# Performance work log

Measured on AMD Instinct MI355X. Metric: run time of the kernel, lower is better.

The kernel has to match this reference:

```python
import jax, jax.numpy as jnp
import numpy as np

D_MODEL = 256
D_STATE = 64
D_CONV = 4
EXPAND = 2
HEADDIM = 64
D_INNER = EXPAND * D_MODEL            # 512
NHEADS = D_INNER // HEADDIM           # 8
D_XBC = D_INNER + 2 * D_STATE         # 640 (x, B, C; ngroups=1)
D_IN_PROJ = 2 * D_INNER + 2 * D_STATE + NHEADS  # 1160


def setup_inputs() -> dict:
    key = jax.random.key(0)
    ks = jax.random.split(key, 8)
    x = jax.random.normal(ks[0], (64, 5000, 12), jnp.float32)
    W_in = jax.random.normal(ks[1], (D_MODEL, D_IN_PROJ), jnp.float32) * 0.02
    conv_w = jax.random.normal(ks[2], (D_XBC, D_CONV), jnp.float32) * 0.1
    conv_b = jnp.zeros((D_XBC,), jnp.float32)
    A_log = jnp.log(jax.random.uniform(ks[3], (NHEADS,), jnp.float32, 1.0, 16.0))
    dt_bias = jax.random.normal(ks[4], (NHEADS,), jnp.float32) * 0.1
    D = jnp.ones((NHEADS,), jnp.float32)
    norm_w = jnp.ones((D_INNER,), jnp.float32)
    W_out = jax.random.normal(ks[5], (D_INNER, D_MODEL), jnp.float32) * 0.02
    return {"x": x, "W_in": W_in, "conv_w": conv_w, "conv_b": conv_b,
            "A_log": A_log, "dt_bias": dt_bias, "D": D,
            "norm_w": norm_w, "W_out": W_out}


def _mamba2(u, W_in, conv_w, conv_b, A_log, dt_bias, D, norm_w, W_out):
    b, l, _ = u.shape
    zxbcdt = u @ W_in                                   # (b,l,1160)
    z = zxbcdt[..., :D_INNER]                           # (b,l,512)
    xBC = zxbcdt[..., D_INNER:D_INNER + D_XBC]          # (b,l,640)
    dt = zxbcdt[..., D_INNER + D_XBC:]                  # (b,l,8)
    # causal depthwise conv1d (kernel 4) + SiLU
    xp = jnp.pad(xBC, ((0, 0), (D_CONV - 1, 0), (0, 0)))
    xBC = sum(xp[:, k:k + l, :] * conv_w[:, k] for k in range(D_CONV)) + conv_b
    xBC = jax.nn.silu(xBC)
    xs = xBC[..., :D_INNER].reshape(b, l, NHEADS, HEADDIM)
    Bm = xBC[..., D_INNER:D_INNER + D_STATE]            # (b,l,64)
    Cm = xBC[..., D_INNER + D_STATE:]                   # (b,l,64)
    dt = jax.nn.softplus(dt + dt_bias)                  # (b,l,h)
    A = -jnp.exp(A_log)                                 # (h,)

    def step(h, inp):
        x_t, dt_t, B_t, C_t = inp                       # (b,h,p),(b,h),(b,n),(b,n)
        decay = jnp.exp(dt_t * A)                       # (b,h)
        h = h * decay[..., None, None] + (dt_t[..., None] * x_t)[..., None] * B_t[:, None, None, :]
        y = jnp.einsum('bhpn,bn->bhp', h, C_t)
        return h, y

    h0 = jnp.zeros((b, NHEADS, HEADDIM, D_STATE), u.dtype)
    _, ys = jax.lax.scan(step, h0, (xs.transpose(1, 0, 2, 3), dt.transpose(1, 0, 2),
                                    Bm.transpose(1, 0, 2), Cm.transpose(1, 0, 2)))
    y = ys.transpose(1, 0, 2, 3) + D[None, None, :, None] * xs   # D skip, per head
    y = y.reshape(b, l, D_INNER)
    # RMSNormGated: gate then rmsnorm
    y = y * jax.nn.silu(z)
    y = y * jax.lax.rsqrt(jnp.mean(y * y, axis=-1, keepdims=True) + 1e-5) * norm_w
    return y @ W_out                                    # (b,l,256)


def reference(x, W_in, conv_w, conv_b, A_log, dt_bias, D, norm_w, W_out):
    b = x.shape[0]
    u = x.reshape(b, 250, 240)                          # 'b (t p1) f -> b t (p1 f)'
    u = jnp.pad(u, ((0, 0), (0, 0), (0, D_MODEL - 240)))
    y = _mamba2(u, W_in, conv_w, conv_b, A_log, dt_bias, D, norm_w, W_out)
    y = jax.nn.selu(y)                                  # AlphaDropout is identity at eval
    y = y[..., :240]
    return y.reshape(b, 5000, 12)
```

## Files before the change

### kernel.cpp

```cpp
#include <hip/hip_runtime.h>
#include <cstdint>
#include <cstddef>

#define D_MODEL 256
#define D_STATE 64
#define HEADDIM 64
#define D_INNER 512
#define NHEADS 8
#define D_XBC 640
#define NPROJ 1160
#define BATCH 64
#define SEQ 250
#define ROWS (BATCH * SEQ)
#define KIN 240
#define KPAD 256
#define NPAD 1216
#define TPAD 256

typedef __bf16 bf16x8 __attribute__((ext_vector_type(8)));
typedef float f32x4 __attribute__((ext_vector_type(4)));

__device__ __forceinline__ float readlane_f(float v, int lane) {
    return __uint_as_float(__builtin_amdgcn_readlane(__float_as_uint(v), lane));
}
__device__ __forceinline__ float silu_f(float x) { return x * (1.f / (1.f + __expf(-x))); }
__device__ __forceinline__ unsigned short bf16_rne(float f) {
    unsigned int u = __float_as_uint(f);
    u += 0x7fff + ((u >> 16) & 1);
    return (unsigned short)(u >> 16);
}
__device__ __forceinline__ float bf2f(unsigned short u) {
    return __uint_as_float(((unsigned int)u) << 16);
}
__device__ __forceinline__ unsigned int pack2(float a, float b) {
    return (unsigned int)bf16_rne(a) | ((unsigned int)bf16_rne(b) << 16);
}

__global__ __launch_bounds__(256) void cast_kernel(const float* __restrict__ x,
                                                   const float* __restrict__ Win,
                                                   unsigned short* __restrict__ a_bf,
                                                   unsigned short* __restrict__ bt_bf) {
    int idx = blockIdx.x * 256 + threadIdx.x;
    const int NA = ROWS * KPAD;
    if (idx < NA) {
        int row = idx >> 8, c = idx & 255;
        float v = (c < KIN) ? x[row * KIN + c] : 0.f;
        a_bf[idx] = bf16_rne(v);
    } else if (idx < NA + NPAD * KPAD) {
        int r = idx - NA;
        int n = r >> 8, k = r & 255;
        float v = (n < NPROJ && k < KIN) ? Win[k * NPROJ + n] : 0.f;
        bt_bf[r] = bf16_rne(v);
    }
}

#define SA 40
__global__ __launch_bounds__(256) void gemm1_mfma(const unsigned short* __restrict__ A,
                                                  const unsigned short* __restrict__ Bt,
                                                  float* __restrict__ C) {
    __shared__ unsigned short As[128 * SA];
    __shared__ unsigned short Bs[64 * SA];
    const int tid = threadIdx.x;
    const int lane = tid & 63, wave = tid >> 6;
    const int wm = wave >> 1, wn = wave & 1;
    const int q = lane >> 4, l15 = lane & 15;
    const int rowBase = blockIdx.y * 128, colBase = blockIdx.x * 64;
    f32x4 acc[4][2] = {};

    const int sr = tid >> 2;
    const int sc = (tid & 3) * 8;

    for (int k0 = 0; k0 < KPAD; k0 += 32) {
        *(float4*)&As[sr * SA + sc] =
            *(const float4*)&A[(size_t)(rowBase + sr) * KPAD + k0 + sc];
        *(float4*)&As[(sr + 64) * SA + sc] =
            *(const float4*)&A[(size_t)(rowBase + sr + 64) * KPAD + k0 + sc];
        *(float4*)&Bs[sr * SA + sc] =
            *(const float4*)&Bt[(size_t)(colBase + sr) * KPAD + k0 + sc];
        __syncthreads();

        bf16x8 bfr[2];
#pragma unroll
        for (int nt = 0; nt < 2; nt++)
            bfr[nt] = *(const bf16x8*)&Bs[(wn * 32 + nt * 16 + l15) * SA + q * 8];
#pragma unroll
        for (int mt = 0; mt < 4; mt++) {
            bf16x8 afr = *(const bf16x8*)&As[(wm * 64 + mt * 16 + l15) * SA + q * 8];
#pragma unroll
            for (int nt = 0; nt < 2; nt++)
                acc[mt][nt] = __builtin_amdgcn_mfma_f32_16x16x32_bf16(afr, bfr[nt],
                                                                      acc[mt][nt], 0, 0, 0);
        }
        __syncthreads();
    }
#pragma unroll
    for (int mt = 0; mt < 4; mt++) {
        int grow = rowBase + wm * 64 + mt * 16 + q * 4;
#pragma unroll
        for (int nt = 0; nt < 2; nt++) {
            int gcol = colBase + wn * 32 + nt * 16 + l15;
            if (gcol < NPROJ) {
#pragma unroll
                for (int reg = 0; reg < 4; reg++)
                    C[(size_t)(grow + reg) * NPROJ + gcol] = acc[mt][nt][reg];
            }
        }
    }
}

#define CT_IN_STR 68
#define CT_TR_STR 70
__global__ __launch_bounds__(256) void conv_kernel(const float* __restrict__ zxbcdt,
                                                   const float* __restrict__ conv_w,
                                                   const float* __restrict__ conv_b,
                                                   const float* __restrict__ dt_bias,
                                                   unsigned short* __restrict__ xc_bf,
                                                   unsigned short* __restrict__ xcT_bf,
                                                   float* __restrict__ dtp) {
    const int b = blockIdx.x;
    const int t0 = blockIdx.z * 64;
    if (blockIdx.y == 10) {
        for (int it = threadIdx.x; it < 512; it += 256) {
            int h = it & 7, ts = it >> 3;
            int t = t0 + (ts << 1);
            t = t0 + (it >> 3);
            if (t < SEQ) {
                float v = zxbcdt[(size_t)(b * SEQ + t) * NPROJ + D_INNER + D_XBC + h] +
                          dt_bias[h];
                dtp[(size_t)(b * SEQ + t) * NHEADS + h] =
                    (v > 20.f) ? v : __logf(1.f + __expf(v));
            }
        }
        return;
    }
    __shared__ float In[67 * CT_IN_STR];
    __shared__ unsigned short OutT[64 * CT_TR_STR];
    const int cg = blockIdx.y;
    const int tid = threadIdx.x;
    const int lane = tid & 63;
    const int w = tid >> 6;
    const int ch = cg * 64 + lane;

    for (int r = w; r < 67; r += 4) {
        int t = t0 - 3 + r;
        float v = (t >= 0 && t < SEQ)
                      ? zxbcdt[(size_t)(b * SEQ + t) * NPROJ + D_INNER + ch]
                      : 0.f;
        In[r * CT_IN_STR + lane] = v;
    }
    __syncthreads();
    const float w0 = conv_w[ch * 4 + 0], w1 = conv_w[ch * 4 + 1];
    const float w2 = conv_w[ch * 4 + 2], w3 = conv_w[ch * 4 + 3];
    const float bias = conv_b[ch];
    unsigned short vals[16];
#pragma unroll
    for (int i = 0; i < 16; i++) {
        int tt = w * 16 + i;
        float acc = fmaf(w3, In[(tt + 3) * CT_IN_STR + lane],
                    fmaf(w2, In[(tt + 2) * CT_IN_STR + lane],
                    fmaf(w1, In[(tt + 1) * CT_IN_STR + lane],
                    fmaf(w0, In[tt * CT_IN_STR + lane], bias))));
        float sv = silu_f(acc);
        unsigned short bv = (t0 + tt < SEQ) ? bf16_rne(sv) : (unsigned short)0;
        vals[i] = bv;
        OutT[lane * CT_TR_STR + tt] = bv;
    }
#pragma unroll
    for (int i = 0; i < 16; i++) {
        int tt = w * 16 + i;
        if (t0 + tt < SEQ)
            xc_bf[(size_t)(b * SEQ + t0 + tt) * D_XBC + ch] = vals[i];
    }
    __syncthreads();
    unsigned short* dstbase = xcT_bf + ((size_t)b * D_XBC + cg * 64) * TPAD + t0;
#pragma unroll
    for (int i = 0; i < 16; i++) {
        int c2 = w * 16 + i;
        dstbase[(size_t)c2 * TPAD + lane] = OutT[c2 * CT_TR_STR + lane];
    }
}

#define LSTR 72
__global__ __launch_bounds__(256) void scan_intra(const unsigned short* __restrict__ xc_bf,
                                                  const unsigned short* __restrict__ xcT_bf,
                                                  const float* __restrict__ dtp,
                                                  const float* __restrict__ A_log,
                                                  const float* __restrict__ Dvec,
                                                  unsigned short* __restrict__ yout_bf,
                                                  unsigned short* __restrict__ st_g) {
    __shared__ unsigned short C_l[64 * LSTR];
    __shared__ unsigned short BP_l[64 * LSTR];
    __shared__ unsigned short XT_l[64 * LSTR];
    __shared__ float cs_s[64], dts_s[64], fws_s[64];

    const int blk = blockIdx.x;
    const int bh = blk >> 2, c = blk & 3;
    const int b = bh >> 3, h = bh & 7;
    const int tid = threadIdx.x;
    const int lane = tid & 63, w = tid >> 6;
    const int q = lane >> 4, l15 = lane & 15;
    const int t0 = c * 64;
    const float A = -__expf(A_log[h]);
    const float Dh = Dvec[h];

    const int r = tid >> 2, c0 = (tid & 3) * 16;

    {
        if (t0 + r < SEQ) {
            const unsigned short* rowp = xc_bf + (size_t)(b * SEQ + t0 + r) * D_XBC;
            *(uint4*)&C_l[r * LSTR + c0] = *(const uint4*)&rowp[D_INNER + D_STATE + c0];
            *(uint4*)&C_l[r * LSTR + c0 + 8] =
                *(const uint4*)&rowp[D_INNER + D_STATE + c0 + 8];
            *(uint4*)&BP_l[r * LSTR + c0] = *(const uint4*)&rowp[D_INNER + c0];
            *(uint4*)&BP_l[r * LSTR + c0 + 8] = *(const uint4*)&rowp[D_INNER + c0 + 8];
        } else {
            uint4 z = {0, 0, 0, 0};
            *(uint4*)&C_l[r * LSTR + c0] = z;
            *(uint4*)&C_l[r * LSTR + c0 + 8] = z;
            *(uint4*)&BP_l[r * LSTR + c0] = z;
            *(uint4*)&BP_l[r * LSTR + c0 + 8] = z;
        }
        const unsigned short* xrow =
            xcT_bf + ((size_t)b * D_XBC + h * HEADDIM + r) * TPAD + t0;
        *(uint4*)&XT_l[r * LSTR + c0] = *(const uint4*)&xrow[c0];
        *(uint4*)&XT_l[r * LSTR + c0 + 8] = *(const uint4*)&xrow[c0 + 8];
    }
    uint4 braw0, braw1;
    {
        const unsigned short* brow =
            xcT_bf + ((size_t)b * D_XBC + D_INNER + r) * TPAD + t0 + c0;
        braw0 = *(const uint4*)&brow[0];
        braw1 = *(const uint4*)&brow[8];
    }
    if (w == 0) {
        int t = lane;
        float dtv = (t0 + t < SEQ) ? dtp[(size_t)(b * SEQ + t0 + t) * NHEADS + h] : 0.f;
        float csv = dtv * A;
#pragma unroll
        for (int o = 1; o < 64; o <<= 1) {
            float u = __shfl_up(csv, o, 64);
            if (lane >= o) csv += u;
        }
        float tot = readlane_f(csv, 63);
        cs_s[t] = csv;
        dts_s[t] = dtv;
        fws_s[t] = dtv * __expf(tot - csv);
    }
    __syncthreads();

    f32x4 g[4] = {};
#pragma unroll
    for (int k0 = 0; k0 < 64; k0 += 32) {
        bf16x8 ca = *(const bf16x8*)&C_l[(w * 16 + l15) * LSTR + k0 + q * 8];
#pragma unroll
        for (int nt = 0; nt < 4; nt++) {
            bf16x8 bb = *(const bf16x8*)&BP_l[(nt * 16 + l15) * LSTR + k0 + q * 8];
            g[nt] = __builtin_amdgcn_mfma_f32_16x16x32_bf16(ca, bb, g[nt], 0, 0, 0);
        }
    }
    __syncthreads();

    {
        unsigned short tmp[16];
        const unsigned short* rp = (const unsigned short*)&braw0;
#pragma unroll
        for (int j = 0; j < 8; j++) tmp[j] = bf16_rne(bf2f(rp[j]) * fws_s[c0 + j]);
        rp = (const unsigned short*)&braw1;
#pragma unroll
        for (int j = 0; j < 8; j++) tmp[8 + j] = bf16_rne(bf2f(rp[j]) * fws_s[c0 + 8 + j]);
        *(uint4*)&C_l[r * LSTR + c0] = *(uint4*)&tmp[0];
        *(uint4*)&C_l[r * LSTR + c0 + 8] = *(uint4*)&tmp[8];
    }
#pragma unroll
    for (int nt = 0; nt < 4; nt++) {
#pragma unroll
        for (int rr = 0; rr < 4; rr++) {
            int t = w * 16 + q * 4 + rr;
            int s = nt * 16 + l15;
            float pv = 0.f;
            if (s <= t) {
                pv = g[nt][rr] * __expf(cs_s[t] - cs_s[s]) * dts_s[s];
                if (s == t) pv += Dh;
            }
            unsigned int u = bf16_rne(pv);
            unsigned int partner = (unsigned int)__shfl_xor((int)u, 1, 64);
            if ((l15 & 1) == 0)
                *(unsigned int*)&BP_l[t * LSTR + nt * 16 + l15] = u | (partner << 16);
        }
    }
    __syncthreads();

    f32x4 y[4] = {};
#pragma unroll
    for (int k0 = 0; k0 < 64; k0 += 32) {
        bf16x8 pa = *(const bf16x8*)&BP_l[(w * 16 + l15) * LSTR + k0 + q * 8];
#pragma unroll
        for (int nt = 0; nt < 4; nt++) {
            bf16x8 xb = *(const bf16x8*)&XT_l[(nt * 16 + l15) * LSTR + k0 + q * 8];
            y[nt] = __builtin_amdgcn_mfma_f32_16x16x32_bf16(pa, xb, y[nt], 0, 0, 0);
        }
    }
    if (c < 3) {
        f32x4 st[4] = {};
#pragma unroll
        for (int k0 = 0; k0 < 64; k0 += 32) {
            bf16x8 xa = *(const bf16x8*)&XT_l[(w * 16 + l15) * LSTR + k0 + q * 8];
#pragma unroll
            for (int nt = 0; nt < 4; nt++) {
                bf16x8 bwb = *(const bf16x8*)&C_l[(nt * 16 + l15) * LSTR + k0 + q * 8];
                st[nt] = __builtin_amdgcn_mfma_f32_16x16x32_bf16(xa, bwb, st[nt], 0, 0, 0);
            }
        }
        unsigned short* stc = st_g + ((size_t)(bh * 3 + c)) * 4096;
#pragma unroll
        for (int nt = 0; nt < 4; nt++)
#pragma unroll
            for (int rr = 0; rr < 4; rr++) {
                unsigned int u = bf16_rne(st[nt][rr]);
                unsigned int partner = (unsigned int)__shfl_xor((int)u, 1, 64);
                if ((l15 & 1) == 0)
                    *(unsigned int*)&stc[(w * 16 + q * 4 + rr) * 64 + nt * 16 + l15] =
                        u | (partner << 16);
            }
    }
#pragma unroll
    for (int nt = 0; nt < 4; nt++)
#pragma unroll
        for (int rr = 0; rr < 4; rr++) {
            int t = w * 16 + q * 4 + rr;
            if (t0 + t < SEQ) {
                int p = nt * 16 + l15;
                unsigned int u = bf16_rne(y[nt][rr]);
                unsigned int partner = (unsigned int)__shfl_xor((int)u, 1, 64);
                if ((l15 & 1) == 0)
                    *(unsigned int*)&yout_bf[(size_t)(b * SEQ + t0 + t) * D_INNER +
                                             h * HEADDIM + p] = u | (partner << 16);
            }
        }
}

__global__ __launch_bounds__(256) void scan_inter(const unsigned short* __restrict__ xc_bf,
                                                  const float* __restrict__ dtp,
                                                  const float* __restrict__ A_log,
                                                  unsigned short* __restrict__ yout_bf,
                                                  const unsigned short* __restrict__ st_g) {
    __shared__ unsigned short C_l[64 * LSTR];
    __shared__ unsigned short h_l[64 * LSTR];
    __shared__ float cs_s[64];
    __shared__ float csum[4];

    const int blk = blockIdx.x;
    const int bh = blk / 3, c = (blk - bh * 3) + 1;
    const int b = bh >> 3, h = bh & 7;
    const int tid = threadIdx.x;
    const int lane = tid & 63, w = tid >> 6;
    const int q = lane >> 4, l15 = lane & 15;
    const int t0 = c * 64;
    const float A = -__expf(A_log[h]);

    {
        int t = lane;
        int gt = w * 64 + t;
        float dtv = (gt < SEQ) ? dtp[(size_t)(b * SEQ + gt) * NHEADS + h] : 0.f;
        float csv = dtv * A;
#pragma unroll
        for (int o = 1; o < 64; o <<= 1) {
            float u = __shfl_up(csv, o, 64);
            if (lane >= o) csv += u;
        }
        if (w == c) cs_s[t] = csv;
        if (lane == 63) csum[w] = csv;
    }
    {
        int r = tid >> 2, c0 = (tid & 3) * 16;
        if (t0 + r < SEQ) {
            const unsigned short* rowp = xc_bf + (size_t)(b * SEQ + t0 + r) * D_XBC;
            *(uint4*)&C_l[r * LSTR + c0] = *(const uint4*)&rowp[D_INNER + D_STATE + c0];
            *(uint4*)&C_l[r * LSTR + c0 + 8] =
                *(const uint4*)&rowp[D_INNER + D_STATE + c0 + 8];
        } else {
            uint4 z = {0, 0, 0, 0};
            *(uint4*)&C_l[r * LSTR + c0] = z;
            *(uint4*)&C_l[r * LSTR + c0 + 8] = z;
        }
    }
    __syncthreads();

    {
        float wgt[3];
        for (int cp = 0; cp < c; cp++) {
            float s = 0.f;
            for (int j = cp + 1; j < c; j++) s += csum[j];
            wgt[cp] = __expf(s);
        }
        const unsigned short* stb = st_g + (size_t)bh * 3 * 4096;
        for (int i = tid; i < 4096; i += 256) {
            float acc = 0.f;
            for (int cp = 0; cp < c; cp++) acc += wgt[cp] * bf2f(stb[cp * 4096 + i]);
            h_l[(i >> 6) * LSTR + (i & 63)] = bf16_rne(acc);
        }
    }
    __syncthreads();

    f32x4 in[4] = {};
#pragma unroll
    for (int k0 = 0; k0 < 64; k0 += 32) {
        bf16x8 ca = *(const bf16x8*)&C_l[(w * 16 + l15) * LSTR + k0 + q * 8];
#pragma unroll
        for (int nt = 0; nt < 4; nt++) {
            bf16x8 hb = *(const bf16x8*)&h_l[(nt * 16 + l15) * LSTR + k0 + q * 8];
            in[nt] = __builtin_amdgcn_mfma_f32_16x16x32_bf16(ca, hb, in[nt], 0, 0, 0);
        }
    }
#pragma unroll
    for (int nt = 0; nt < 4; nt++)
#pragma unroll
        for (int r = 0; r < 4; r++) {
            int t = w * 16 + q * 4 + r;
            if (t0 + t < SEQ) {
                int p = nt * 16 + l15;
                size_t ai = (size_t)(b * SEQ + t0 + t) * D_INNER + h * HEADDIM + p;
                float alpha = __expf(cs_s[t]);
                float nv = bf2f(yout_bf[ai]) + alpha * in[nt][r];
                unsigned int u = bf16_rne(nv);
                unsigned int partner = (unsigned int)__shfl_xor((int)u, 1, 64);
                if ((l15 & 1) == 0)
                    *(unsigned int*)&yout_bf[ai] = u | (partner << 16);
            }
        }
}

__global__ __launch_bounds__(256) void wcast_kernel(const float* __restrict__ Wout,
                                                    unsigned short* __restrict__ wt_bf) {
    int idx = blockIdx.x * 256 + threadIdx.x;
    int n = idx & 255, k = idx >> 8;
    wt_bf[n * D_INNER + k] = bf16_rne(Wout[k * D_MODEL + n]);
}

__global__ __launch_bounds__(256) void gate_kernel(const unsigned short* __restrict__ yout_bf,
                                                   const float* __restrict__ zx,
                                                   const float* __restrict__ norm_w,
                                                   unsigned short* __restrict__ g_bf) {
    const int wid = threadIdx.x >> 6, lane = threadIdx.x & 63;
    const int row = blockIdx.x * 4 + wid;
    const unsigned short* yr = yout_bf + (size_t)row * D_INNER;
    const float* zr = zx + (size_t)row * NPROJ;
    const int c0 = lane * 8;
    uint4 yp = *(const uint4*)&yr[c0];
    float4 z0 = *(const float4*)&zr[c0], z1 = *(const float4*)&zr[c0 + 4];
    float g[8];
    g[0] = bf2f((unsigned short)(yp.x & 0xffff)) * silu_f(z0.x);
    g[1] = bf2f((unsigned short)(yp.x >> 16)) * silu_f(z0.y);
    g[2] = bf2f((unsigned short)(yp.y & 0xffff)) * silu_f(z0.z);
    g[3] = bf2f((unsigned short)(yp.y >> 16)) * silu_f(z0.w);
    g[4] = bf2f((unsigned short)(yp.z & 0xffff)) * silu_f(z1.x);
    g[5] = bf2f((unsigned short)(yp.z >> 16)) * silu_f(z1.y);
    g[6] = bf2f((unsigned short)(yp.w & 0xffff)) * silu_f(z1.z);
    g[7] = bf2f((unsigned short)(yp.w >> 16)) * silu_f(z1.w);
    float s = 0.f;
#pragma unroll
    for (int i = 0; i < 8; i++) s = fmaf(g[i], g[i], s);
#pragma unroll
    for (int o = 32; o; o >>= 1) s += __shfl_xor(s, o, 64);
    float rms = rsqrtf(s * (1.f / 512.f) + 1e-5f);
    float4 w0 = *(const float4*)&norm_w[c0], w1 = *(const float4*)&norm_w[c0 + 4];
    uint4 pk;
    pk.x = pack2(g[0] * rms * w0.x, g[1] * rms * w0.y);
    pk.y = pack2(g[2] * rms * w0.z, g[3] * rms * w0.w);
    pk.z = pack2(g[4] * rms * w1.x, g[5] * rms * w1.y);
    pk.w = pack2(g[6] * rms * w1.z, g[7] * rms * w1.w);
    *(uint4*)&g_bf[(size_t)row * D_INNER + c0] = pk;
}

__global__ __launch_bounds__(256) void gemm2_mfma(const unsigned short* __restrict__ A,
                                                  const unsigned short* __restrict__ Bt,
                                                  float* __restrict__ out) {
    __shared__ unsigned short As[128 * SA];
    __shared__ unsigned short Bs[64 * SA];
    const int tid = threadIdx.x;
    const int lane = tid & 63, wave = tid >> 6;
    const int wm = wave >> 1, wn = wave & 1;
    const int q = lane >> 4, l15 = lane & 15;
    const int rowBase = blockIdx.y * 128, colBase = blockIdx.x * 64;
    f32x4 acc[4][2] = {};

    const int sr = tid >> 2;
    const int sc = (tid & 3) * 8;

    for (int k0 = 0; k0 < D_INNER; k0 += 32) {
        *(float4*)&As[sr * SA + sc] =
            *(const float4*)&A[(size_t)(rowBase + sr) * D_INNER + k0 + sc];
        *(float4*)&As[(sr + 64) * SA + sc] =
            *(const float4*)&A[(size_t)(rowBase + sr + 64) * D_INNER + k0 + sc];
        *(float4*)&Bs[sr * SA + sc] =
            *(const float4*)&Bt[(size_t)(colBase + sr) * D_INNER + k0 + sc];
        __syncthreads();

        bf16x8 bfr[2];
#pragma unroll
        for (int nt = 0; nt < 2; nt++)
            bfr[nt] = *(const bf16x8*)&Bs[(wn * 32 + nt * 16 + l15) * SA + q * 8];
#pragma unroll
        for (int mt = 0; mt < 4; mt++) {
            bf16x8 afr = *(const bf16x8*)&As[(wm * 64 + mt * 16 + l15) * SA + q * 8];
#pragma unroll
            for (int nt = 0; nt < 2; nt++)
                acc[mt][nt] = __builtin_amdgcn_mfma_f32_16x16x32_bf16(afr, bfr[nt],
                                                                      acc[mt][nt], 0, 0, 0);
        }
        __syncthreads();
    }
    const float SC = 1.0507009873554805f, AL = 1.6732632423543772f;
#pragma unroll
    for (int mt = 0; mt < 4; mt++) {
        int grow = rowBase + wm * 64 + mt * 16 + q * 4;
#pragma unroll
        for (int nt = 0; nt < 2; nt++) {
            int gcol = colBase + wn * 32 + nt * 16 + l15;
            if (gcol < 240) {
#pragma unroll
                for (int reg = 0; reg < 4; reg++) {
                    float v = acc[mt][nt][reg];
                    v = (v > 0.f) ? SC * v : SC * AL * (__expf(v) - 1.f);
                    out[(size_t)(grow + reg) * 240 + gcol] = v;
                }
            }
        }
    }
}

extern "C" void kernel_launch(void* const* d_in, const int* in_sizes, int n_in,
                              void* d_out, int out_size, void* d_ws, size_t ws_size,
                              hipStream_t stream) {
    const float* x = (const float*)d_in[0];
    const float* W_in = (const float*)d_in[1];
    const float* conv_w = (const float*)d_in[2];
    const float* conv_b = (const float*)d_in[3];
    const float* A_log = (const float*)d_in[4];
    const float* dt_bias = (const float*)d_in[5];
    const float* Dv = (const float*)d_in[6];
    const float* norm_w = (const float*)d_in[7];
    const float* W_out = (const float*)d_in[8];
    float* out = (float*)d_out;

    float* ws = (float*)d_ws;
    float* zxbcdt = ws;
    unsigned short* xc_bf = (unsigned short*)(zxbcdt + (size_t)ROWS * NPROJ);
    unsigned short* xcT_bf = xc_bf + (size_t)ROWS * D_XBC;
    float* dtp = (float*)(xcT_bf + (size_t)BATCH * D_XBC * TPAD);
    unsigned short* yout_bf = (unsigned short*)(dtp + (size_t)ROWS * NHEADS);
    unsigned short* st_g = yout_bf + (size_t)ROWS * D_INNER;

    unsigned short* a_bf = xc_bf;
    unsigned short* bt_bf = a_bf + (size_t)ROWS * KPAD;
    unsigned short* wt_bf = (unsigned short*)dtp;
    unsigned short* g_bf = xc_bf;

    int cast_total = ROWS * KPAD + NPAD * KPAD;
    cast_kernel<<<dim3((cast_total + 255) / 256), 256, 0, stream>>>(x, W_in, a_bf, bt_bf);

    gemm1_mfma<<<dim3(NPAD / 64, ROWS / 128), 256, 0, stream>>>(a_bf, bt_bf, zxbcdt);

    conv_kernel<<<dim3(BATCH, 11, 4), 256, 0, stream>>>(zxbcdt, conv_w, conv_b, dt_bias,
                                                        xc_bf, xcT_bf, dtp);

    scan_intra<<<dim3(BATCH * NHEADS * 4), 256, 0, stream>>>(xc_bf, xcT_bf, dtp, A_log, Dv,
                                                             yout_bf, st_g);

    scan_inter<<<dim3(BATCH * NHEADS * 3), 256, 0, stream>>>(xc_bf, dtp, A_log,
                                                             yout_bf, st_g);

    wcast_kernel<<<dim3(D_INNER * D_MODEL / 256), 256, 0, stream>>>(W_out, wt_bf);

    gate_kernel<<<dim3(ROWS / 4), 256, 0, stream>>>(yout_bf, zxbcdt, norm_w, g_bf);

    gemm2_mfma<<<dim3(D_MODEL / 64, ROWS / 128), 256, 0, stream>>>(g_bf, wt_bf, out);
}
```

Baseline: 222.6 us.

## Fuse input cast into GEMM1 and store projection output as bf16

Drops the separate activation cast kernel: GEMM1 now reads the fp32 input directly and converts it to bf16 while staging into shared memory, zero-padding K beyond 240. The z/xBC part of the projection output is written as packed bf16 with row stride 1152, and the dt columns go to a separate small fp32 buffer. Conv and gate kernels are changed to read the bf16 tensor. This roughly halves the intermediate write and read traffic, at the cost of bf16 rounding of z and xBC before conv and gating, plus a lane shuffle in the GEMM epilogue.

```diff
diff --git a/kernel.cpp b/kernel.cpp
--- a/kernel.cpp
+++ b/kernel.cpp
@@ -9,6 +9,7 @@
 #define NHEADS 8
 #define D_XBC 640
 #define NPROJ 1160
+#define ZXW 1152
 #define BATCH 64
 #define SEQ 250
 #define ROWS (BATCH * SEQ)
@@ -36,28 +37,19 @@
     return (unsigned int)bf16_rne(a) | ((unsigned int)bf16_rne(b) << 16);
 }
 
-__global__ __launch_bounds__(256) void cast_kernel(const float* __restrict__ x,
-                                                   const float* __restrict__ Win,
-                                                   unsigned short* __restrict__ a_bf,
-                                                   unsigned short* __restrict__ bt_bf) {
+__global__ __launch_bounds__(256) void cast_w_kernel(const float* __restrict__ Win,
+                                                     unsigned short* __restrict__ bt_bf) {
     int idx = blockIdx.x * 256 + threadIdx.x;
-    const int NA = ROWS * KPAD;
-    if (idx < NA) {
-        int row = idx >> 8, c = idx & 255;
-        float v = (c < KIN) ? x[row * KIN + c] : 0.f;
-        a_bf[idx] = bf16_rne(v);
-    } else if (idx < NA + NPAD * KPAD) {
-        int r = idx - NA;
-        int n = r >> 8, k = r & 255;
-        float v = (n < NPROJ && k < KIN) ? Win[k * NPROJ + n] : 0.f;
-        bt_bf[r] = bf16_rne(v);
-    }
+    int n = idx >> 8, k = idx & 255;
+    float v = (n < NPROJ && k < KIN) ? Win[k * NPROJ + n] : 0.f;
+    bt_bf[idx] = bf16_rne(v);
 }
 
 #define SA 40
-__global__ __launch_bounds__(256) void gemm1_mfma(const unsigned short* __restrict__ A,
+__global__ __launch_bounds__(256) void gemm1_mfma(const float* __restrict__ X,
                                                   const unsigned short* __restrict__ Bt,
-                                                  float* __restrict__ C) {
+                                                  unsigned short* __restrict__ Czx,
+                                                  float* __restrict__ dtraw) {
     __shared__ unsigned short As[128 * SA];
     __shared__ unsigned short Bs[64 * SA];
     const int tid = threadIdx.x;
@@ -71,10 +63,34 @@
     const int sc = (tid & 3) * 8;
 
     for (int k0 = 0; k0 < KPAD; k0 += 32) {
-        *(float4*)&As[sr * SA + sc] =
-            *(const float4*)&A[(size_t)(rowBase + sr) * KPAD + k0 + sc];
-        *(float4*)&As[(sr + 64) * SA + sc] =
-            *(const float4*)&A[(size_t)(rowBase + sr + 64) * KPAD + k0 + sc];
+        const int kseg = k0 + sc;
+        const bool kv = kseg < KIN;
+        {
+            unsigned short tmp[8] = {0, 0, 0, 0, 0, 0, 0, 0};
+            if (kv) {
+                const float* xr = X + (size_t)(rowBase + sr) * KIN + kseg;
+                float4 a = *(const float4*)&xr[0];
+                float4 b2 = *(const float4*)&xr[4];
+                tmp[0] = bf16_rne(a.x); tmp[1] = bf16_rne(a.y);
+                tmp[2] = bf16_rne(a.z); tmp[3] = bf16_rne(a.w);
+                tmp[4] = bf16_rne(b2.x); tmp[5] = bf16_rne(b2.y);
+                tmp[6] = bf16_rne(b2.z); tmp[7] = bf16_rne(b2.w);
+            }
+            *(uint4*)&As[sr * SA + sc] = *(uint4*)tmp;
+        }
+        {
+            unsigned short tmp[8] = {0, 0, 0, 0, 0, 0, 0, 0};
+            if (kv) {
+                const float* xr = X + (size_t)(rowBase + sr + 64) * KIN + kseg;
+                float4 a = *(const float4*)&xr[0];
+                float4 b2 = *(const float4*)&xr[4];
+                tmp[0] = bf16_rne(a.x); tmp[1] = bf16_rne(a.y);
+                tmp[2] = bf16_rne(a.z); tmp[3] = bf16_rne(a.w);
+                tmp[4] = bf16_rne(b2.x); tmp[5] = bf16_rne(b2.y);
+                tmp[6] = bf16_rne(b2.z); tmp[7] = bf16_rne(b2.w);
+            }
+            *(uint4*)&As[(sr + 64) * SA + sc] = *(uint4*)tmp;
+        }
         *(float4*)&Bs[sr * SA + sc] =
             *(const float4*)&Bt[(size_t)(colBase + sr) * KPAD + k0 + sc];
         __syncthreads();
@@ -95,14 +111,23 @@
     }
 #pragma unroll
     for (int mt = 0; mt < 4; mt++) {
-        int grow = rowBase + wm * 64 + mt * 16 + q * 4;
+        int grow0 = rowBase + wm * 64 + mt * 16 + q * 4;
 #pragma unroll
         for (int nt = 0; nt < 2; nt++) {
             int gcol = colBase + wn * 32 + nt * 16 + l15;
-            if (gcol < NPROJ) {
+            if (gcol < ZXW) {
+#pragma unroll
+                for (int reg = 0; reg < 4; reg++) {
+                    unsigned int u = bf16_rne(acc[mt][nt][reg]);
+                    unsigned int partner = (unsigned int)__shfl_xor((int)u, 1, 64);
+                    if ((l15 & 1) == 0)
+                        *(unsigned int*)&Czx[(size_t)(grow0 + reg) * ZXW + gcol] =
+                            u | (partner << 16);
+                }
+            } else if (gcol < NPROJ) {
 #pragma unroll
                 for (int reg = 0; reg < 4; reg++)
-                    C[(size_t)(grow + reg) * NPROJ + gcol] = acc[mt][nt][reg];
+                    dtraw[(size_t)(grow0 + reg) * NHEADS + (gcol - ZXW)] = acc[mt][nt][reg];
             }
         }
     }
@@ -110,7 +135,8 @@
 
 #define CT_IN_STR 68
 #define CT_TR_STR 70
-__global__ __launch_bounds__(256) void conv_kernel(const float* __restrict__ zxbcdt,
+__global__ __launch_bounds__(256) void conv_kernel(const unsigned short* __restrict__ zxbc,
+                                                   const float* __restrict__ dtraw,
                                                    const float* __restrict__ conv_w,
                                                    const float* __restrict__ conv_b,
                                                    const float* __restrict__ dt_bias,
@@ -121,12 +147,10 @@
     const int t0 = blockIdx.z * 64;
     if (blockIdx.y == 10) {
         for (int it = threadIdx.x; it < 512; it += 256) {
-            int h = it & 7, ts = it >> 3;
-            int t = t0 + (ts << 1);
-            t = t0 + (it >> 3);
+            int h = it & 7;
+            int t = t0 + (it >> 3);
             if (t < SEQ) {
-                float v = zxbcdt[(size_t)(b * SEQ + t) * NPROJ + D_INNER + D_XBC + h] +
-                          dt_bias[h];
+                float v = dtraw[(size_t)(b * SEQ + t) * NHEADS + h] + dt_bias[h];
                 dtp[(size_t)(b * SEQ + t) * NHEADS + h] =
                     (v > 20.f) ? v : __logf(1.f + __expf(v));
             }
@@ -144,7 +168,7 @@
     for (int r = w; r < 67; r += 4) {
         int t = t0 - 3 + r;
         float v = (t >= 0 && t < SEQ)
-                      ? zxbcdt[(size_t)(b * SEQ + t) * NPROJ + D_INNER + ch]
+                      ? bf2f(zxbc[(size_t)(b * SEQ + t) * ZXW + D_INNER + ch])
                       : 0.f;
         In[r * CT_IN_STR + lane] = v;
     }
@@ -438,25 +462,21 @@
 }
 
 __global__ __launch_bounds__(256) void gate_kernel(const unsigned short* __restrict__ yout_bf,
-                                                   const float* __restrict__ zx,
+                                                   const unsigned short* __restrict__ zxbc,
                                                    const float* __restrict__ norm_w,
                                                    unsigned short* __restrict__ g_bf) {
     const int wid = threadIdx.x >> 6, lane = threadIdx.x & 63;
     const int row = blockIdx.x * 4 + wid;
     const unsigned short* yr = yout_bf + (size_t)row * D_INNER;
-    const float* zr = zx + (size_t)row * NPROJ;
+    const unsigned short* zr = zxbc + (size_t)row * ZXW;
     const int c0 = lane * 8;
     uint4 yp = *(const uint4*)&yr[c0];
-    float4 z0 = *(const float4*)&zr[c0], z1 = *(const float4*)&zr[c0 + 4];
+    uint4 zp = *(const uint4*)&zr[c0];
+    const unsigned short* ys = (const unsigned short*)&yp;
+    const unsigned short* zs = (const unsigned short*)&zp;
     float g[8];
-    g[0] = bf2f((unsigned short)(yp.x & 0xffff)) * silu_f(z0.x);
-    g[1] = bf2f((unsigned short)(yp.x >> 16)) * silu_f(z0.y);
-    g[2] = bf2f((unsigned short)(yp.y & 0xffff)) * silu_f(z0.z);
-    g[3] = bf2f((unsigned short)(yp.y >> 16)) * silu_f(z0.w);
-    g[4] = bf2f((unsigned short)(yp.z & 0xffff)) * silu_f(z1.x);
-    g[5] = bf2f((unsigned short)(yp.z >> 16)) * silu_f(z1.y);
-    g[6] = bf2f((unsigned short)(yp.w & 0xffff)) * silu_f(z1.z);
-    g[7] = bf2f((unsigned short)(yp.w >> 16)) * silu_f(z1.w);
+#pragma unroll
+    for (int i = 0; i < 8; i++) g[i] = bf2f(ys[i]) * silu_f(bf2f(zs[i]));
     float s = 0.f;
 #pragma unroll
     for (int i = 0; i < 8; i++) s = fmaf(g[i], g[i], s);
@@ -543,26 +563,24 @@
     const float* W_out = (const float*)d_in[8];
     float* out = (float*)d_out;
 
-    float* ws = (float*)d_ws;
-    float* zxbcdt = ws;
-    unsigned short* xc_bf = (unsigned short*)(zxbcdt + (size_t)ROWS * NPROJ);
+    unsigned short* us = (unsigned short*)d_ws;
+    unsigned short* zxbc_bf = us;
+    unsigned short* xc_bf = zxbc_bf + (size_t)ROWS * ZXW;
     unsigned short* xcT_bf = xc_bf + (size_t)ROWS * D_XBC;
-    float* dtp = (float*)(xcT_bf + (size_t)BATCH * D_XBC * TPAD);
-    unsigned short* yout_bf = (unsigned short*)(dtp + (size_t)ROWS * NHEADS);
+    unsigned short* yout_bf = xcT_bf + (size_t)BATCH * D_XBC * TPAD;
     unsigned short* st_g = yout_bf + (size_t)ROWS * D_INNER;
-
-    unsigned short* a_bf = xc_bf;
-    unsigned short* bt_bf = a_bf + (size_t)ROWS * KPAD;
-    unsigned short* wt_bf = (unsigned short*)dtp;
-    unsigned short* g_bf = xc_bf;
-
-    int cast_total = ROWS * KPAD + NPAD * KPAD;
-    cast_kernel<<<dim3((cast_total + 255) / 256), 256, 0, stream>>>(x, W_in, a_bf, bt_bf);
-
-    gemm1_mfma<<<dim3(NPAD / 64, ROWS / 128), 256, 0, stream>>>(a_bf, bt_bf, zxbcdt);
-
-    conv_kernel<<<dim3(BATCH, 11, 4), 256, 0, stream>>>(zxbcdt, conv_w, conv_b, dt_bias,
-                                                        xc_bf, xcT_bf, dtp);
+    unsigned short* bt_bf = st_g + (size_t)512 * 3 * 4096;
+    unsigned short* wt_bf = bt_bf + (size_t)NPAD * KPAD;
+    unsigned short* g_bf = wt_bf + (size_t)D_MODEL * D_INNER;
+    float* dtraw = (float*)(g_bf + (size_t)ROWS * D_INNER);
+    float* dtp = dtraw + (size_t)ROWS * NHEADS;
+
+    cast_w_kernel<<<dim3(NPAD * KPAD / 256), 256, 0, stream>>>(W_in, bt_bf);
+
+    gemm1_mfma<<<dim3(NPAD / 64, ROWS / 128), 256, 0, stream>>>(x, bt_bf, zxbc_bf, dtraw);
+
+    conv_kernel<<<dim3(BATCH, 11, 4), 256, 0, stream>>>(zxbc_bf, dtraw, conv_w, conv_b,
+                                                        dt_bias, xc_bf, xcT_bf, dtp);
 
     scan_intra<<<dim3(BATCH * NHEADS * 4), 256, 0, stream>>>(xc_bf, xcT_bf, dtp, A_log, Dv,
                                                              yout_bf, st_g);
@@ -572,7 +590,7 @@
 
     wcast_kernel<<<dim3(D_INNER * D_MODEL / 256), 256, 0, stream>>>(W_out, wt_bf);
 
-    gate_kernel<<<dim3(ROWS / 4), 256, 0, stream>>>(yout_bf, zxbcdt, norm_w, g_bf);
+    gate_kernel<<<dim3(ROWS / 4), 256, 0, stream>>>(yout_bf, zxbc_bf, norm_w, g_bf);
 
     gemm2_mfma<<<dim3(D_MODEL / 64, ROWS / 128), 256, 0, stream>>>(g_bf, wt_bf, out);
 }
```

After: 221.6 us. Within noise of the previous version (-0.5%).
